# Performance work log

Measured on AMD Instinct MI355X. Metric: run time of the kernel, lower is better.

The kernel has to match this reference:

```python
import jax, jax.numpy as jnp
import numpy as np
from math import sqrt

SCALE = sqrt(512.0)  # max(key_size, attn_hidden_size, query_size) with scaled=True

def setup_inputs() -> dict:
    key = jax.random.key(0)
    k1, k2, k3, k4, k5 = jax.random.split(key, 5)
    B, T, S, M, N, H = 8, 512, 512, 512, 512, 128
    return {
        "query": jax.random.normal(k1, (B, T, M), dtype=jnp.float32),
        "keys": jax.random.normal(k2, (B, S, N), dtype=jnp.float32),
        "W1": jax.random.normal(k3, (N, H), dtype=jnp.float32),
        "W2": jax.random.normal(k4, (M, H), dtype=jnp.float32),
        "v": jax.random.normal(k5, (H,), dtype=jnp.float32),
    }

def reference(query, keys, W1, W2, v):
    # Project query and keys into attention hidden space
    x1 = jnp.einsum('btm,mh->bth', query, W2)   # (B,T,H)
    x2 = jnp.einsum('bsn,nh->bsh', keys, W1)    # (B,S,H)
    # Broadcast merge (op='add'), tanh activation, v-weighted reduction over H
    merged = jnp.tanh(x1[:, :, None, :] + x2[:, None, :, :])  # (B,T,S,H)
    score = jnp.einsum('btsh,h->bts', merged, v)
    return score / SCALE
```

## Files before the change

### kernel.cpp

```cpp
#include <hip/hip_runtime.h>
#include <hip/hip_fp16.h>


constexpr float SCALE_IN  = 2.8853900817779268f;
constexpr float INV_SCALE = 0.04419417382415922f;

__global__ __launch_bounds__(512) void proj_kernel(
    const float* __restrict__ q,  const float* __restrict__ w2,
    const float* __restrict__ ky, const float* __restrict__ w1,
    unsigned int* __restrict__ x1w, unsigned int* __restrict__ x2w) {
  __shared__ float As[32 * 64];
  __shared__ float Ws[64 * 128];

  int blk = blockIdx.x;
  const float* A; const float* W; unsigned int* O;
  if (blk < 128) { A = q;  W = w2; O = x1w; }
  else           { blk -= 128; A = ky; W = w1; O = x2w; }
  const int rbase = blk * 32;
  const int tid = threadIdx.x;

  const int rq = tid >> 5;
  const int hq = tid & 31;

  float acc[2][4];
#pragma unroll
  for (int r = 0; r < 2; ++r)
#pragma unroll
    for (int c = 0; c < 4; ++c) acc[r][c] = 0.0f;

  for (int kb = 0; kb < 512; kb += 64) {
    {
      const int arow = tid >> 4;
      const int kq4  = (tid & 15) * 4;
      *(float4*)(As + arow * 64 + kq4) =
          *(const float4*)(A + (size_t)(rbase + arow) * 512 + kb + kq4);
      const int wrow = tid >> 5;
      const int hq4  = (tid & 31) * 4;
#pragma unroll
      for (int p = 0; p < 4; ++p)
        *(float4*)(Ws + (wrow + 16 * p) * 128 + hq4) =
            *(const float4*)(W + (size_t)(kb + wrow + 16 * p) * 128 + hq4);
    }
    __syncthreads();
#pragma unroll 4
    for (int k4 = 0; k4 < 64; k4 += 4) {
      float a[2][4], w[4][4];
      *(float4*)a[0] = *(const float4*)(As + (2 * rq + 0) * 64 + k4);
      *(float4*)a[1] = *(const float4*)(As + (2 * rq + 1) * 64 + k4);
#pragma unroll
      for (int kk = 0; kk < 4; ++kk)
        *(float4*)w[kk] = *(const float4*)(Ws + (k4 + kk) * 128 + 4 * hq);
#pragma unroll
      for (int kk = 0; kk < 4; ++kk)
#pragma unroll
        for (int r = 0; r < 2; ++r)
#pragma unroll
          for (int c = 0; c < 4; ++c)
            acc[r][c] = fmaf(a[r][kk], w[kk][c], acc[r][c]);
    }
    __syncthreads();
  }

#pragma unroll
  for (int r = 0; r < 2; ++r) {
    unsigned int pk[4];
#pragma unroll
    for (int c = 0; c < 4; ++c) {
      const float z  = acc[r][c] * SCALE_IN;
      const float kf = rintf(z);
      const int   ki = (int)kf;
      const float em = __builtin_amdgcn_exp2f(z - kf);
      const __half hh = __float2half_rn(em);
      pk[c] = ((unsigned int)ki << 16) | (unsigned int)__half_as_ushort(hh);
    }
    *(uint4*)(O + (size_t)(rbase + 2 * rq + r) * 128 + 4 * hq) = *(uint4*)pk;
  }
}

__global__ __launch_bounds__(512) void score_kernel(
    const unsigned int* __restrict__ x1w, const unsigned int* __restrict__ x2w,
    const float* __restrict__ v, float* __restrict__ out) {
  __shared__ unsigned int x1l[128 * 64];
  __shared__ unsigned int x2l[128 * 64];

  const int tid   = threadIdx.x;
  const int b     = blockIdx.x >> 6;
  const int tile  = blockIdx.x & 63;
  const int tbase = (tile >> 3) * 64;
  const int sbase = (tile & 7) * 64;

  const uint4* x1g = (const uint4*)(x1w + (b * 512 + tbase) * 128);
  const uint4* x2g = (const uint4*)(x2w + (b * 512 + sbase) * 128);

  const int l  = tid & 63;
  const int wq = tid >> 6;
#pragma unroll
  for (int p = 0; p < 4; ++p) {
    const int row = (l & 31) + 32 * (p & 1);
    const int c4  = (l >> 5) + 2 * wq + 16 * (p >> 1);
    const uint4 a = x1g[row * 32 + c4];
    x1l[(4 * c4 + 0) * 64 + row] = a.x;
    x1l[(4 * c4 + 1) * 64 + row] = a.y;
    x1l[(4 * c4 + 2) * 64 + row] = a.z;
    x1l[(4 * c4 + 3) * 64 + row] = a.w;
    const uint4 c = x2g[row * 32 + c4];
    x2l[(4 * c4 + 0) * 64 + row] = c.x;
    x2l[(4 * c4 + 1) * 64 + row] = c.y;
    x2l[(4 * c4 + 2) * 64 + row] = c.z;
    x2l[(4 * c4 + 3) * 64 + row] = c.w;
  }
  __syncthreads();

  const int sg = tid & 15;
  const int tg = tid >> 4;

  float racc[2][4];
#pragma unroll
  for (int i = 0; i < 2; ++i)
#pragma unroll
    for (int j = 0; j < 4; ++j) racc[i][j] = 0.0f;
  float sv = 0.0f;

  for (int hg = 0; hg < 32; ++hg) {
    const int h0 = hg * 4;
    const float4 vq = *(const float4*)(v + h0);
    sv += (vq.x + vq.y) + (vq.z + vq.w);

    float emt[2][4]; int kt[2][4];
    float ems[4][4]; int ks[4][4];
#pragma unroll
    for (int qq = 0; qq < 4; ++qq) {
      const uint2 tp = *(const uint2*)(x1l + (h0 + qq) * 64 + 2 * tg);
      emt[0][qq] = __half2float(__ushort_as_half((unsigned short)tp.x));
      kt [0][qq] = ((int)tp.x) >> 16;
      emt[1][qq] = __half2float(__ushort_as_half((unsigned short)tp.y));
      kt [1][qq] = ((int)tp.y) >> 16;
      const uint4 sp = *(const uint4*)(x2l + (h0 + qq) * 64 + 4 * sg);
      ems[0][qq] = __half2float(__ushort_as_half((unsigned short)sp.x));
      ks [0][qq] = ((int)sp.x) >> 16;
      ems[1][qq] = __half2float(__ushort_as_half((unsigned short)sp.y));
      ks [1][qq] = ((int)sp.y) >> 16;
      ems[2][qq] = __half2float(__ushort_as_half((unsigned short)sp.z));
      ks [2][qq] = ((int)sp.z) >> 16;
      ems[3][qq] = __half2float(__ushort_as_half((unsigned short)sp.w));
      ks [3][qq] = ((int)sp.w) >> 16;
    }

#pragma unroll
    for (int i = 0; i < 2; ++i) {
#pragma unroll
      for (int j = 0; j < 4; ++j) {
        float e[4];
#pragma unroll
        for (int qq = 0; qq < 4; ++qq) {
          int kk = kt[i][qq] + ks[j][qq];
          kk = min(kk, 30);
          e[qq] = ldexpf(emt[i][qq] * ems[j][qq], kk);
        }
        const float a0 = e[0] + 1.0f, a1 = e[1] + 1.0f;
        const float a2 = e[2] + 1.0f, a3 = e[3] + 1.0f;
        const float p12 = a0 * a1, p34 = a2 * a3;
        float u1 = vq.x * a1; u1 = fmaf(vq.y, a0, u1);
        float u2 = vq.z * a3; u2 = fmaf(vq.w, a2, u2);
        float num = u1 * p34; num = fmaf(u2, p12, num);
        const float den = p12 * p34;
        racc[i][j] = fmaf(num, __builtin_amdgcn_rcpf(den), racc[i][j]);
      }
    }
  }

  const float c1 = sv * INV_SCALE;
  const float c2 = -2.0f * INV_SCALE;
#pragma unroll
  for (int i = 0; i < 2; ++i) {
    const int t = tbase + 2 * tg + i;
    float4 o;
    o.x = fmaf(racc[i][0], c2, c1);
    o.y = fmaf(racc[i][1], c2, c1);
    o.z = fmaf(racc[i][2], c2, c1);
    o.w = fmaf(racc[i][3], c2, c1);
    *(float4*)(out + (size_t)(b * 512 + t) * 512 + sbase + 4 * sg) = o;
  }
}

extern "C" void kernel_launch(void* const* d_in, const int* in_sizes, int n_in,
                              void* d_out, int out_size, void* d_ws, size_t ws_size,
                              hipStream_t stream) {
  const float* query = (const float*)d_in[0];
  const float* keys  = (const float*)d_in[1];
  const float* W1    = (const float*)d_in[2];
  const float* W2    = (const float*)d_in[3];
  const float* v     = (const float*)d_in[4];
  float* out = (float*)d_out;

  unsigned int* x1w = (unsigned int*)d_ws;
  unsigned int* x2w = x1w + 8 * 512 * 128;

  hipLaunchKernelGGL(proj_kernel, dim3(256), dim3(512), 0, stream,
                     query, W2, keys, W1, x1w, x2w);
  hipLaunchKernelGGL(score_kernel, dim3(512), dim3(512), 0, stream,
                     x1w, x2w, v, out);
}
```

Baseline: 147.1 us.

## Split projection K across blocks, add pack kernel, shrink score tiles

The projection GEMM is split into two K-halves, doubling its grid to 512 blocks. The fp32 partials are written into the output buffer as scratch, and a new pack kernel sums them and encodes the exp2 mantissa/exponent pairs. The score kernel now uses 64x32 tiles across 1024 blocks, stages H in two 64-wide phases to halve LDS use, and sets launch bounds for 8 waves per SIMD. The aim is more parallelism and occupancy on the many CUs, at the cost of an extra launch, extra global round-trips for partials, and less per-thread register reuse.

```diff
diff --git a/kernel.cpp b/kernel.cpp
--- a/kernel.cpp
+++ b/kernel.cpp
@@ -5,17 +5,18 @@
 constexpr float SCALE_IN  = 2.8853900817779268f;
 constexpr float INV_SCALE = 0.04419417382415922f;
 
-__global__ __launch_bounds__(512) void proj_kernel(
+__global__ __launch_bounds__(512) void proj_partial_kernel(
     const float* __restrict__ q,  const float* __restrict__ w2,
     const float* __restrict__ ky, const float* __restrict__ w1,
-    unsigned int* __restrict__ x1w, unsigned int* __restrict__ x2w) {
+    float* __restrict__ part) {
   __shared__ float As[32 * 64];
   __shared__ float Ws[64 * 128];
 
-  int blk = blockIdx.x;
-  const float* A; const float* W; unsigned int* O;
-  if (blk < 128) { A = q;  W = w2; O = x1w; }
-  else           { blk -= 128; A = ky; W = w1; O = x2w; }
+  const int khalf = blockIdx.x >> 8;
+  int blk = blockIdx.x & 255;
+  const float* A; const float* W; int mat;
+  if (blk < 128) { A = q;  W = w2; mat = 0; }
+  else           { blk -= 128; A = ky; W = w1; mat = 1; }
   const int rbase = blk * 32;
   const int tid = threadIdx.x;
 
@@ -28,7 +29,8 @@
 #pragma unroll
     for (int c = 0; c < 4; ++c) acc[r][c] = 0.0f;
 
-  for (int kb = 0; kb < 512; kb += 64) {
+  const int k0 = khalf * 256;
+  for (int kb = k0; kb < k0 + 256; kb += 64) {
     {
       const int arow = tid >> 4;
       const int kq4  = (tid & 15) * 4;
@@ -61,125 +63,134 @@
     __syncthreads();
   }
 
-#pragma unroll
-  for (int r = 0; r < 2; ++r) {
-    unsigned int pk[4];
-#pragma unroll
-    for (int c = 0; c < 4; ++c) {
-      const float z  = acc[r][c] * SCALE_IN;
-      const float kf = rintf(z);
-      const int   ki = (int)kf;
-      const float em = __builtin_amdgcn_exp2f(z - kf);
-      const __half hh = __float2half_rn(em);
-      pk[c] = ((unsigned int)ki << 16) | (unsigned int)__half_as_ushort(hh);
-    }
-    *(uint4*)(O + (size_t)(rbase + 2 * rq + r) * 128 + 4 * hq) = *(uint4*)pk;
-  }
-}
-
-__global__ __launch_bounds__(512) void score_kernel(
+  float* O = part + (size_t)(mat * 2 + khalf) * (4096 * 128);
+#pragma unroll
+  for (int r = 0; r < 2; ++r)
+    *(float4*)(O + (size_t)(rbase + 2 * rq + r) * 128 + 4 * hq) =
+        *(float4*)acc[r];
+}
+
+__global__ __launch_bounds__(256) void pack_kernel(
+    const float4* __restrict__ part, uint4* __restrict__ o1,
+    uint4* __restrict__ o2) {
+  const int t = blockIdx.x * 256 + threadIdx.x;
+  const int m = t >> 17;
+  const int e = t & 131071;
+  const float4 p0 = part[(size_t)(m * 2 + 0) * 131072 + e];
+  const float4 p1 = part[(size_t)(m * 2 + 1) * 131072 + e];
+  const float x[4] = {p0.x + p1.x, p0.y + p1.y, p0.z + p1.z, p0.w + p1.w};
+  unsigned int pk[4];
+#pragma unroll
+  for (int c = 0; c < 4; ++c) {
+    const float z  = x[c] * SCALE_IN;
+    const float kf = rintf(z);
+    const int   ki = (int)kf;
+    const float em = __builtin_amdgcn_exp2f(z - kf);
+    pk[c] = ((unsigned int)ki << 16) |
+            (unsigned int)__half_as_ushort(__float2half_rn(em));
+  }
+  (m == 0 ? o1 : o2)[e] = *(const uint4*)pk;
+}
+
+__global__ __launch_bounds__(512, 8) void score_kernel(
     const unsigned int* __restrict__ x1w, const unsigned int* __restrict__ x2w,
     const float* __restrict__ v, float* __restrict__ out) {
-  __shared__ unsigned int x1l[128 * 64];
-  __shared__ unsigned int x2l[128 * 64];
+  __shared__ unsigned int x1l[64 * 64];
+  __shared__ unsigned int x2l[64 * 32];
 
   const int tid   = threadIdx.x;
-  const int b     = blockIdx.x >> 6;
-  const int tile  = blockIdx.x & 63;
-  const int tbase = (tile >> 3) * 64;
-  const int sbase = (tile & 7) * 64;
-
-  const uint4* x1g = (const uint4*)(x1w + (b * 512 + tbase) * 128);
-  const uint4* x2g = (const uint4*)(x2w + (b * 512 + sbase) * 128);
-
-  const int l  = tid & 63;
-  const int wq = tid >> 6;
-#pragma unroll
-  for (int p = 0; p < 4; ++p) {
-    const int row = (l & 31) + 32 * (p & 1);
-    const int c4  = (l >> 5) + 2 * wq + 16 * (p >> 1);
-    const uint4 a = x1g[row * 32 + c4];
-    x1l[(4 * c4 + 0) * 64 + row] = a.x;
-    x1l[(4 * c4 + 1) * 64 + row] = a.y;
-    x1l[(4 * c4 + 2) * 64 + row] = a.z;
-    x1l[(4 * c4 + 3) * 64 + row] = a.w;
-    const uint4 c = x2g[row * 32 + c4];
-    x2l[(4 * c4 + 0) * 64 + row] = c.x;
-    x2l[(4 * c4 + 1) * 64 + row] = c.y;
-    x2l[(4 * c4 + 2) * 64 + row] = c.z;
-    x2l[(4 * c4 + 3) * 64 + row] = c.w;
-  }
-  __syncthreads();
+  const int b     = blockIdx.x >> 7;
+  const int tile  = blockIdx.x & 127;
+  const int tbase = (tile >> 4) * 64;
+  const int sbase = (tile & 15) * 32;
+
+  const uint4* x1g = (const uint4*)(x1w) + (size_t)(b * 512 + tbase) * 32;
+  const uint4* x2g = (const uint4*)(x2w) + (size_t)(b * 512 + sbase) * 32;
 
   const int sg = tid & 15;
   const int tg = tid >> 4;
 
-  float racc[2][4];
-#pragma unroll
-  for (int i = 0; i < 2; ++i)
-#pragma unroll
-    for (int j = 0; j < 4; ++j) racc[i][j] = 0.0f;
+  float racc[2][2] = {{0.0f, 0.0f}, {0.0f, 0.0f}};
   float sv = 0.0f;
 
-  for (int hg = 0; hg < 32; ++hg) {
-    const int h0 = hg * 4;
-    const float4 vq = *(const float4*)(v + h0);
-    sv += (vq.x + vq.y) + (vq.z + vq.w);
-
-    float emt[2][4]; int kt[2][4];
-    float ems[4][4]; int ks[4][4];
-#pragma unroll
-    for (int qq = 0; qq < 4; ++qq) {
-      const uint2 tp = *(const uint2*)(x1l + (h0 + qq) * 64 + 2 * tg);
-      emt[0][qq] = __half2float(__ushort_as_half((unsigned short)tp.x));
-      kt [0][qq] = ((int)tp.x) >> 16;
-      emt[1][qq] = __half2float(__ushort_as_half((unsigned short)tp.y));
-      kt [1][qq] = ((int)tp.y) >> 16;
-      const uint4 sp = *(const uint4*)(x2l + (h0 + qq) * 64 + 4 * sg);
-      ems[0][qq] = __half2float(__ushort_as_half((unsigned short)sp.x));
-      ks [0][qq] = ((int)sp.x) >> 16;
-      ems[1][qq] = __half2float(__ushort_as_half((unsigned short)sp.y));
-      ks [1][qq] = ((int)sp.y) >> 16;
-      ems[2][qq] = __half2float(__ushort_as_half((unsigned short)sp.z));
-      ks [2][qq] = ((int)sp.z) >> 16;
-      ems[3][qq] = __half2float(__ushort_as_half((unsigned short)sp.w));
-      ks [3][qq] = ((int)sp.w) >> 16;
-    }
-
-#pragma unroll
-    for (int i = 0; i < 2; ++i) {
-#pragma unroll
-      for (int j = 0; j < 4; ++j) {
-        float e[4];
-#pragma unroll
-        for (int qq = 0; qq < 4; ++qq) {
-          int kk = kt[i][qq] + ks[j][qq];
-          kk = min(kk, 30);
-          e[qq] = ldexpf(emt[i][qq] * ems[j][qq], kk);
+  for (int ph = 0; ph < 2; ++ph) {
+    {
+      const int t1 = tid & 63;
+      const int c1 = tid >> 6;
+#pragma unroll
+      for (int p = 0; p < 2; ++p) {
+        const int c4 = c1 + 8 * p;
+        const uint4 a = x1g[t1 * 32 + ph * 16 + c4];
+        x1l[(4 * c4 + 0) * 64 + t1] = a.x;
+        x1l[(4 * c4 + 1) * 64 + t1] = a.y;
+        x1l[(4 * c4 + 2) * 64 + t1] = a.z;
+        x1l[(4 * c4 + 3) * 64 + t1] = a.w;
+      }
+      const int s1 = tid & 31;
+      const int c2 = tid >> 5;
+      const uint4 c = x2g[s1 * 32 + ph * 16 + c2];
+      x2l[(4 * c2 + 0) * 32 + s1] = c.x;
+      x2l[(4 * c2 + 1) * 32 + s1] = c.y;
+      x2l[(4 * c2 + 2) * 32 + s1] = c.z;
+      x2l[(4 * c2 + 3) * 32 + s1] = c.w;
+    }
+    __syncthreads();
+
+    for (int hg = 0; hg < 16; ++hg) {
+      const int h0 = hg * 4;
+      const float4 vq = *(const float4*)(v + ph * 64 + h0);
+      sv += (vq.x + vq.y) + (vq.z + vq.w);
+
+      float emt[2][4]; int kt[2][4];
+      float ems[2][4]; int ks[2][4];
+#pragma unroll
+      for (int qq = 0; qq < 4; ++qq) {
+        const uint2 tp = *(const uint2*)(x1l + (h0 + qq) * 64 + 2 * tg);
+        emt[0][qq] = __half2float(__ushort_as_half((unsigned short)tp.x));
+        kt [0][qq] = ((int)tp.x) >> 16;
+        emt[1][qq] = __half2float(__ushort_as_half((unsigned short)tp.y));
+        kt [1][qq] = ((int)tp.y) >> 16;
+        const uint2 sp = *(const uint2*)(x2l + (h0 + qq) * 32 + 2 * sg);
+        ems[0][qq] = __half2float(__ushort_as_half((unsigned short)sp.x));
+        ks [0][qq] = ((int)sp.x) >> 16;
+        ems[1][qq] = __half2float(__ushort_as_half((unsigned short)sp.y));
+        ks [1][qq] = ((int)sp.y) >> 16;
+      }
+
+#pragma unroll
+      for (int i = 0; i < 2; ++i) {
+#pragma unroll
+        for (int j = 0; j < 2; ++j) {
+          float e[4];
+#pragma unroll
+          for (int qq = 0; qq < 4; ++qq) {
+            int kk = kt[i][qq] + ks[j][qq];
+            kk = min(kk, 30);
+            e[qq] = ldexpf(emt[i][qq] * ems[j][qq], kk);
+          }
+          const float a0 = e[0] + 1.0f, a1 = e[1] + 1.0f;
+          const float a2 = e[2] + 1.0f, a3 = e[3] + 1.0f;
+          const float p12 = a0 * a1, p34 = a2 * a3;
+          float u1 = vq.x * a1; u1 = fmaf(vq.y, a0, u1);
+          float u2 = vq.z * a3; u2 = fmaf(vq.w, a2, u2);
+          float num = u1 * p34; num = fmaf(u2, p12, num);
+          const float den = p12 * p34;
+          racc[i][j] = fmaf(num, __builtin_amdgcn_rcpf(den), racc[i][j]);
         }
-        const float a0 = e[0] + 1.0f, a1 = e[1] + 1.0f;
-        const float a2 = e[2] + 1.0f, a3 = e[3] + 1.0f;
-        const float p12 = a0 * a1, p34 = a2 * a3;
-        float u1 = vq.x * a1; u1 = fmaf(vq.y, a0, u1);
-        float u2 = vq.z * a3; u2 = fmaf(vq.w, a2, u2);
-        float num = u1 * p34; num = fmaf(u2, p12, num);
-        const float den = p12 * p34;
-        racc[i][j] = fmaf(num, __builtin_amdgcn_rcpf(den), racc[i][j]);
       }
     }
-  }
-
-  const float c1 = sv * INV_SCALE;
-  const float c2 = -2.0f * INV_SCALE;
+    __syncthreads();
+  }
+
+  const float c1v = sv * INV_SCALE;
+  const float c2v = -2.0f * INV_SCALE;
 #pragma unroll
   for (int i = 0; i < 2; ++i) {
     const int t = tbase + 2 * tg + i;
-    float4 o;
-    o.x = fmaf(racc[i][0], c2, c1);
-    o.y = fmaf(racc[i][1], c2, c1);
-    o.z = fmaf(racc[i][2], c2, c1);
-    o.w = fmaf(racc[i][3], c2, c1);
-    *(float4*)(out + (size_t)(b * 512 + t) * 512 + sbase + 4 * sg) = o;
+    float2 o;
+    o.x = fmaf(racc[i][0], c2v, c1v);
+    o.y = fmaf(racc[i][1], c2v, c1v);
+    *(float2*)(out + (size_t)(b * 512 + t) * 512 + sbase + 2 * sg) = o;
   }
 }
 
@@ -196,8 +207,12 @@
   unsigned int* x1w = (unsigned int*)d_ws;
   unsigned int* x2w = x1w + 8 * 512 * 128;
 
-  hipLaunchKernelGGL(proj_kernel, dim3(256), dim3(512), 0, stream,
-                     query, W2, keys, W1, x1w, x2w);
-  hipLaunchKernelGGL(score_kernel, dim3(512), dim3(512), 0, stream,
+  float* part = (float*)d_out;
+
+  hipLaunchKernelGGL(proj_partial_kernel, dim3(512), dim3(512), 0, stream,
+                     query, W2, keys, W1, part);
+  hipLaunchKernelGGL(pack_kernel, dim3(1024), dim3(256), 0, stream,
+                     (const float4*)part, (uint4*)x1w, (uint4*)x2w);
+  hipLaunchKernelGGL(score_kernel, dim3(1024), dim3(512), 0, stream,
                      x1w, x2w, v, out);
 }
```

Measured after the change: 149.8 us. About the same (+1.8%).

## Pack exponent in fp32 mantissa bits and halve score-kernel LDS via two H phases

Applied to the files above, without the earlier changes.

The projection output now keeps the fp32 mantissa of exp2(frac) and stores a clamped 10-bit exponent in its low mantissa bits, replacing the half-plus-16-bit-exponent packing. The score kernel then unpacks with a bitcast and shift instead of half-to-float conversions. The score kernel also stages H in two 64-wide phases, halving LDS per block, and adds a min-blocks launch bound so more blocks can be resident. The costs are an extra synchronisation round per phase and a small precision change from truncating the mantissa.

```diff
diff --git a/kernel.cpp b/kernel.cpp
--- a/kernel.cpp
+++ b/kernel.cpp
@@ -68,20 +68,20 @@
     for (int c = 0; c < 4; ++c) {
       const float z  = acc[r][c] * SCALE_IN;
       const float kf = rintf(z);
-      const int   ki = (int)kf;
+      int ki = (int)kf;
+      ki = max(min(ki, 511), -512);
       const float em = __builtin_amdgcn_exp2f(z - kf);
-      const __half hh = __float2half_rn(em);
-      pk[c] = ((unsigned int)ki << 16) | (unsigned int)__half_as_ushort(hh);
+      pk[c] = (__float_as_uint(em) & 0xFFFFFC00u) | ((unsigned int)ki & 1023u);
     }
     *(uint4*)(O + (size_t)(rbase + 2 * rq + r) * 128 + 4 * hq) = *(uint4*)pk;
   }
 }
 
-__global__ __launch_bounds__(512) void score_kernel(
+__global__ __launch_bounds__(512, 4) void score_kernel(
     const unsigned int* __restrict__ x1w, const unsigned int* __restrict__ x2w,
     const float* __restrict__ v, float* __restrict__ out) {
-  __shared__ unsigned int x1l[128 * 64];
-  __shared__ unsigned int x2l[128 * 64];
+  __shared__ unsigned int x1l[64 * 64];
+  __shared__ unsigned int x2l[64 * 64];
 
   const int tid   = threadIdx.x;
   const int b     = blockIdx.x >> 6;
@@ -89,27 +89,8 @@
   const int tbase = (tile >> 3) * 64;
   const int sbase = (tile & 7) * 64;
 
-  const uint4* x1g = (const uint4*)(x1w + (b * 512 + tbase) * 128);
-  const uint4* x2g = (const uint4*)(x2w + (b * 512 + sbase) * 128);
-
-  const int l  = tid & 63;
-  const int wq = tid >> 6;
-#pragma unroll
-  for (int p = 0; p < 4; ++p) {
-    const int row = (l & 31) + 32 * (p & 1);
-    const int c4  = (l >> 5) + 2 * wq + 16 * (p >> 1);
-    const uint4 a = x1g[row * 32 + c4];
-    x1l[(4 * c4 + 0) * 64 + row] = a.x;
-    x1l[(4 * c4 + 1) * 64 + row] = a.y;
-    x1l[(4 * c4 + 2) * 64 + row] = a.z;
-    x1l[(4 * c4 + 3) * 64 + row] = a.w;
-    const uint4 c = x2g[row * 32 + c4];
-    x2l[(4 * c4 + 0) * 64 + row] = c.x;
-    x2l[(4 * c4 + 1) * 64 + row] = c.y;
-    x2l[(4 * c4 + 2) * 64 + row] = c.z;
-    x2l[(4 * c4 + 3) * 64 + row] = c.w;
-  }
-  __syncthreads();
+  const unsigned int* x1g = x1w + (size_t)(b * 512 + tbase) * 128;
+  const unsigned int* x2g = x2w + (size_t)(b * 512 + sbase) * 128;
 
   const int sg = tid & 15;
   const int tg = tid >> 4;
@@ -121,64 +102,89 @@
     for (int j = 0; j < 4; ++j) racc[i][j] = 0.0f;
   float sv = 0.0f;
 
-  for (int hg = 0; hg < 32; ++hg) {
-    const int h0 = hg * 4;
-    const float4 vq = *(const float4*)(v + h0);
-    sv += (vq.x + vq.y) + (vq.z + vq.w);
-
-    float emt[2][4]; int kt[2][4];
-    float ems[4][4]; int ks[4][4];
-#pragma unroll
-    for (int qq = 0; qq < 4; ++qq) {
-      const uint2 tp = *(const uint2*)(x1l + (h0 + qq) * 64 + 2 * tg);
-      emt[0][qq] = __half2float(__ushort_as_half((unsigned short)tp.x));
-      kt [0][qq] = ((int)tp.x) >> 16;
-      emt[1][qq] = __half2float(__ushort_as_half((unsigned short)tp.y));
-      kt [1][qq] = ((int)tp.y) >> 16;
-      const uint4 sp = *(const uint4*)(x2l + (h0 + qq) * 64 + 4 * sg);
-      ems[0][qq] = __half2float(__ushort_as_half((unsigned short)sp.x));
-      ks [0][qq] = ((int)sp.x) >> 16;
-      ems[1][qq] = __half2float(__ushort_as_half((unsigned short)sp.y));
-      ks [1][qq] = ((int)sp.y) >> 16;
-      ems[2][qq] = __half2float(__ushort_as_half((unsigned short)sp.z));
-      ks [2][qq] = ((int)sp.z) >> 16;
-      ems[3][qq] = __half2float(__ushort_as_half((unsigned short)sp.w));
-      ks [3][qq] = ((int)sp.w) >> 16;
-    }
-
-#pragma unroll
-    for (int i = 0; i < 2; ++i) {
-#pragma unroll
-      for (int j = 0; j < 4; ++j) {
-        float e[4];
-#pragma unroll
-        for (int qq = 0; qq < 4; ++qq) {
-          int kk = kt[i][qq] + ks[j][qq];
-          kk = min(kk, 30);
-          e[qq] = ldexpf(emt[i][qq] * ems[j][qq], kk);
+  for (int ph = 0; ph < 2; ++ph) {
+    {
+      const int r1 = tid & 63;
+      const int c0 = tid >> 6;
+#pragma unroll
+      for (int p = 0; p < 2; ++p) {
+        const int c = c0 + 8 * p;
+        const uint4 a =
+            *(const uint4*)(x1g + (size_t)r1 * 128 + ph * 64 + 4 * c);
+        x1l[(4 * c + 0) * 64 + r1] = a.x;
+        x1l[(4 * c + 1) * 64 + r1] = a.y;
+        x1l[(4 * c + 2) * 64 + r1] = a.z;
+        x1l[(4 * c + 3) * 64 + r1] = a.w;
+        const uint4 s =
+            *(const uint4*)(x2g + (size_t)r1 * 128 + ph * 64 + 4 * c);
+        x2l[(4 * c + 0) * 64 + r1] = s.x;
+        x2l[(4 * c + 1) * 64 + r1] = s.y;
+        x2l[(4 * c + 2) * 64 + r1] = s.z;
+        x2l[(4 * c + 3) * 64 + r1] = s.w;
+      }
+    }
+    __syncthreads();
+
+    for (int hg = 0; hg < 16; ++hg) {
+      const int h0 = hg * 4;
+      const float4 vq = *(const float4*)(v + ph * 64 + h0);
+      sv += (vq.x + vq.y) + (vq.z + vq.w);
+
+      float emt[2][4]; int kt[2][4];
+      float ems[4][4]; int ks[4][4];
+#pragma unroll
+      for (int qq = 0; qq < 4; ++qq) {
+        const uint2 tp = *(const uint2*)(x1l + (h0 + qq) * 64 + 2 * tg);
+        emt[0][qq] = __uint_as_float(tp.x);
+        kt [0][qq] = (int)(tp.x << 22) >> 22;
+        emt[1][qq] = __uint_as_float(tp.y);
+        kt [1][qq] = (int)(tp.y << 22) >> 22;
+        const uint4 sp = *(const uint4*)(x2l + (h0 + qq) * 64 + 4 * sg);
+        ems[0][qq] = __uint_as_float(sp.x);
+        ks [0][qq] = (int)(sp.x << 22) >> 22;
+        ems[1][qq] = __uint_as_float(sp.y);
+        ks [1][qq] = (int)(sp.y << 22) >> 22;
+        ems[2][qq] = __uint_as_float(sp.z);
+        ks [2][qq] = (int)(sp.z << 22) >> 22;
+        ems[3][qq] = __uint_as_float(sp.w);
+        ks [3][qq] = (int)(sp.w << 22) >> 22;
+      }
+
+#pragma unroll
+      for (int i = 0; i < 2; ++i) {
+#pragma unroll
+        for (int j = 0; j < 4; ++j) {
+          float e[4];
+#pragma unroll
+          for (int qq = 0; qq < 4; ++qq) {
+            int kk = kt[i][qq] + ks[j][qq];
+            kk = min(kk, 30);
+            e[qq] = ldexpf(emt[i][qq] * ems[j][qq], kk);
+          }
+          const float a0 = e[0] + 1.0f, a1 = e[1] + 1.0f;
+          const float a2 = e[2] + 1.0f, a3 = e[3] + 1.0f;
+          const float p12 = a0 * a1, p34 = a2 * a3;
+          float u1 = vq.x * a1; u1 = fmaf(vq.y, a0, u1);
+          float u2 = vq.z * a3; u2 = fmaf(vq.w, a2, u2);
+          float num = u1 * p34; num = fmaf(u2, p12, num);
+          const float den = p12 * p34;
+          racc[i][j] = fmaf(num, __builtin_amdgcn_rcpf(den), racc[i][j]);
         }
-        const float a0 = e[0] + 1.0f, a1 = e[1] + 1.0f;
-        const float a2 = e[2] + 1.0f, a3 = e[3] + 1.0f;
-        const float p12 = a0 * a1, p34 = a2 * a3;
-        float u1 = vq.x * a1; u1 = fmaf(vq.y, a0, u1);
-        float u2 = vq.z * a3; u2 = fmaf(vq.w, a2, u2);
-        float num = u1 * p34; num = fmaf(u2, p12, num);
-        const float den = p12 * p34;
-        racc[i][j] = fmaf(num, __builtin_amdgcn_rcpf(den), racc[i][j]);
       }
     }
-  }
-
-  const float c1 = sv * INV_SCALE;
-  const float c2 = -2.0f * INV_SCALE;
+    __syncthreads();
+  }
+
+  const float c1v = sv * INV_SCALE;
+  const float c2v = -2.0f * INV_SCALE;
 #pragma unroll
   for (int i = 0; i < 2; ++i) {
     const int t = tbase + 2 * tg + i;
     float4 o;
-    o.x = fmaf(racc[i][0], c2, c1);
-    o.y = fmaf(racc[i][1], c2, c1);
-    o.z = fmaf(racc[i][2], c2, c1);
-    o.w = fmaf(racc[i][3], c2, c1);
+    o.x = fmaf(racc[i][0], c2v, c1v);
+    o.y = fmaf(racc[i][1], c2v, c1v);
+    o.z = fmaf(racc[i][2], c2v, c1v);
+    o.w = fmaf(racc[i][3], c2v, c1v);
     *(float4*)(out + (size_t)(b * 512 + t) * 512 + sbase + 4 * sg) = o;
   }
 }
```

Result: no change. 146.1 us (-0.6%).
